# Kernel optimization log

Measured on AMD Instinct MI355X. Metric: run time of the kernel, lower is better.

Reference implementation:

```python
import jax, jax.numpy as jnp
import numpy as np

N_NODES = 50000
DROP_P = 0.2


def gcn_conv(x, edge_index, W, b):
    """PyG GCNConv: add self-loops, symmetric D^-1/2 (A+I) D^-1/2 normalization."""
    n = x.shape[0]
    loop = jnp.arange(n, dtype=edge_index.dtype)
    src = jnp.concatenate([edge_index[0], loop])  # [E+N]
    dst = jnp.concatenate([edge_index[1], loop])  # [E+N]
    # degree over destination (incl. self loop), all edge weights = 1
    deg = jax.ops.segment_sum(jnp.ones_like(src, dtype=x.dtype), dst, num_segments=n)
    dinv = jnp.where(deg > 0, jax.lax.rsqrt(deg), 0.0)
    norm = dinv[src] * dinv[dst]  # [E+N]
    h = x @ W  # [N, F_out] transform first (PyG order)
    msg = h[src] * norm[:, None]  # gather + scale
    out = jax.ops.segment_sum(msg, dst, num_segments=n)  # scatter-add
    return out + b


def setup_inputs() -> dict:
    key = jax.random.key(0)
    ks = jax.random.split(key, 4)
    x = jax.random.normal(ks[0], (N_NODES, 512), dtype=jnp.float32)
    edge_index = jax.random.randint(ks[1], (2, 800000), 0, N_NODES, dtype=jnp.int64)
    W1 = jax.random.normal(ks[2], (512, 256), dtype=jnp.float32) * (1.0 / np.sqrt(512))
    b1 = jnp.zeros((256,), dtype=jnp.float32)
    W2 = jax.random.normal(ks[3], (256, 128), dtype=jnp.float32) * (1.0 / np.sqrt(256))
    b2 = jnp.zeros((128,), dtype=jnp.float32)
    return {"x": x, "edge_index": edge_index, "W1": W1, "b1": b1, "W2": W2, "b2": b2}


def reference(x, edge_index, W1, b1, W2, b2):
    h = gcn_conv(x, edge_index, W1, b1)
    h = jax.nn.relu(h)
    # F.dropout(p=0.2) with training=True default; deterministic fixed-key mask
    keep = jax.random.bernoulli(jax.random.key(42), 1.0 - DROP_P, h.shape)
    h = jnp.where(keep, h / (1.0 - DROP_P), 0.0)
    h = gcn_conv(h, edge_index, W2, b2)
    return jax.nn.softmax(h, axis=1)
```

## Files before the change

kernel.cpp:

```cpp
#include <hip/hip_runtime.h>
#include <stdint.h>

#define N_NODES 50000
#define N_EDGES 800000
#define F0 512
#define F1 256
#define F2 128
#define CAP 64

typedef __attribute__((ext_vector_type(8))) short short8;
typedef __attribute__((ext_vector_type(4))) float float4v;

__device__ __forceinline__ uint32_t r8_rotl(uint32_t x, int r) {
    return (x << r) | (x >> (32 - r));
}

__device__ __forceinline__ uint32_t r8_bits32(uint32_t idx) {
    const uint32_t ks0 = 0u;
    const uint32_t ks1 = 42u;
    const uint32_t ks2 = 0x1BD11BDAu ^ ks0 ^ ks1;
    uint32_t x0 = ks0;
    uint32_t x1 = idx + ks1;
#define R8R(r) { x0 += x1; x1 = r8_rotl(x1, (r)); x1 ^= x0; }
    R8R(13) R8R(15) R8R(26) R8R(6)
    x0 += ks1; x1 += ks2 + 1u;
    R8R(17) R8R(29) R8R(16) R8R(24)
    x0 += ks2; x1 += ks0 + 2u;
    R8R(13) R8R(15) R8R(26) R8R(6)
    x0 += ks0; x1 += ks1 + 3u;
    R8R(17) R8R(29) R8R(16) R8R(24)
    x0 += ks1; x1 += ks2 + 4u;
    R8R(13) R8R(15) R8R(26) R8R(6)
    x0 += ks2; x1 += ks0 + 5u;
#undef R8R
    return x0 ^ x1;
}

__device__ __forceinline__ int r8_keep(uint32_t idx) {
    return (r8_bits32(idx) >> 9) < 0x666667u;
}

__device__ __forceinline__ unsigned short r8_f2bf(float f) {
    uint32_t u = __float_as_uint(f);
    uint32_t r = u + 0x7fffu + ((u >> 16) & 1u);
    return (unsigned short)(r >> 16);
}

__global__ void r8_detect(const uint32_t* __restrict__ ei, int* __restrict__ flag) {
    int t = threadIdx.x;
    uint32_t v = ei[2 * t + 1] | ei[128 + 2 * t + 1];
    unsigned long long any_nonzero = __ballot(v != 0u);
    if (t == 0) flag[0] = (any_nonzero == 0ull) ? 1 : 0;
}

__global__ void r8_fill(const int* __restrict__ ei, const int* __restrict__ flag,
                        int* __restrict__ cursor, int* __restrict__ bucket) {
    int e = blockIdx.x * 256 + threadIdx.x;
    if (e < N_EDGES) {
        int f = flag[0];
        int s = ei[(size_t)e << f];
        int d = ei[(size_t)(N_EDGES + e) << f];
        int pos = atomicAdd(&cursor[d], 1);
        if (pos < CAP) bucket[(size_t)d * CAP + pos] = s;
    }
}

__global__ void r8_dinv(const int* __restrict__ cursor, float* __restrict__ dinv) {
    int v = blockIdx.x * 256 + threadIdx.x;
    if (v < N_NODES) dinv[v] = 1.0f / sqrtf((float)(cursor[v] + 1));
}

__global__ void r8_w1t(const float* __restrict__ W1, unsigned short* __restrict__ Bt) {
    int k = blockIdx.x;
    int n = threadIdx.x;
    Bt[(size_t)n * F0 + k] = r8_f2bf(W1[(size_t)k * F1 + n]);
}

__global__ void r8_w2t(const float* __restrict__ W2, unsigned short* __restrict__ Bt) {
    int k = blockIdx.x;
    int n = threadIdx.x;
    Bt[(size_t)n * F1 + k] = r8_f2bf(W2[(size_t)k * F2 + n]);
}

#define G1_LDA 40
__global__ __launch_bounds__(512)
void r8_gemm1(const float* __restrict__ A, const unsigned short* __restrict__ Bt,
              unsigned short* __restrict__ C, int M) {
    __shared__ unsigned short As[2][128][G1_LDA];
    __shared__ unsigned short Bs[2][256][G1_LDA];
    const int bm = blockIdx.x * 128;
    const int tid = threadIdx.x;
    const int wave = tid >> 6;
    const int lane = tid & 63;
    const int wm = (wave & 1) * 64;
    const int wn = (wave >> 1) * 64;
    const int l15 = lane & 15;
    const int quad = lane >> 4;

    const int asr = tid >> 2;
    const int ask = (tid & 3) * 8;
    const int bsr = tid >> 1;
    const int bsk = (tid & 1) * 16;

    float4v acc[4][4];
#pragma unroll
    for (int i = 0; i < 4; ++i)
#pragma unroll
        for (int j = 0; j < 4; ++j) acc[i][j] = (float4v){0.f, 0.f, 0.f, 0.f};

    const int arow = bm + asr;
    const bool avalid = arow < M;
    const float* aptr = A + (size_t)(avalid ? arow : 0) * F0 + ask;
    const unsigned short* bptr = Bt + (size_t)bsr * F0 + bsk;

    float4 apfA[2], apfB[2];
    short8 bpfA[2], bpfB[2];
#pragma unroll
    for (int q = 0; q < 2; ++q) {
        apfA[q] = make_float4(0.f, 0.f, 0.f, 0.f);
        apfB[q] = make_float4(0.f, 0.f, 0.f, 0.f);
    }

    auto load_tile = [&](int kt, float4 (&apf)[2], short8 (&bpf)[2]) {
        const int k0 = kt * 32;
        if (avalid) {
            const float4* ap = (const float4*)(aptr + k0);
            apf[0] = ap[0];
            apf[1] = ap[1];
        }
        bpf[0] = *(const short8*)(bptr + k0);
        bpf[1] = *(const short8*)(bptr + k0 + 8);
    };

    auto write_buf = [&](int buf, const float4 (&apf)[2], const short8 (&bpf)[2]) {
        union { short8 v; unsigned short u[8]; } t;
        t.u[0] = r8_f2bf(apf[0].x); t.u[1] = r8_f2bf(apf[0].y);
        t.u[2] = r8_f2bf(apf[0].z); t.u[3] = r8_f2bf(apf[0].w);
        t.u[4] = r8_f2bf(apf[1].x); t.u[5] = r8_f2bf(apf[1].y);
        t.u[6] = r8_f2bf(apf[1].z); t.u[7] = r8_f2bf(apf[1].w);
        *(short8*)&As[buf][asr][ask] = t.v;
        *(short8*)&Bs[buf][bsr][bsk] = bpf[0];
        *(short8*)&Bs[buf][bsr][bsk + 8] = bpf[1];
    };

    auto compute = [&](int cur) {
        short8 afr[4], bfr[4];
#pragma unroll
        for (int mi = 0; mi < 4; ++mi)
            afr[mi] = *(const short8*)&As[cur][wm + mi * 16 + l15][quad * 8];
#pragma unroll
        for (int ni = 0; ni < 4; ++ni)
            bfr[ni] = *(const short8*)&Bs[cur][wn + ni * 16 + l15][quad * 8];
#pragma unroll
        for (int mi = 0; mi < 4; ++mi)
#pragma unroll
            for (int ni = 0; ni < 4; ++ni)
                acc[mi][ni] = __builtin_amdgcn_mfma_f32_16x16x32_bf16(
                    afr[mi], bfr[ni], acc[mi][ni], 0, 0, 0);
    };

    const int NT = F0 / 32;
    load_tile(0, apfA, bpfA);
    write_buf(0, apfA, bpfA);
    load_tile(1, apfB, bpfB);
    __syncthreads();

    for (int kt = 0; kt < NT; kt += 2) {
        if (kt + 2 < NT) load_tile(kt + 2, apfA, bpfA);
        compute(0);
        write_buf(1, apfB, bpfB);
        __syncthreads();
        if (kt + 3 < NT) load_tile(kt + 3, apfB, bpfB);
        compute(1);
        if (kt + 2 < NT) write_buf(0, apfA, bpfA);
        __syncthreads();
    }

#pragma unroll
    for (int mi = 0; mi < 4; ++mi) {
#pragma unroll
        for (int r = 0; r < 4; ++r) {
            int row = bm + wm + mi * 16 + quad * 4 + r;
            if (row < M) {
                unsigned short* cp = C + (size_t)row * F1 + wn + l15;
#pragma unroll
                for (int ni = 0; ni < 4; ++ni) cp[ni * 16] = r8_f2bf(acc[mi][ni][r]);
            }
        }
    }
}

#define G2_LDA 40
__global__ __launch_bounds__(256)
void r8_gemm2(const unsigned short* __restrict__ A, const unsigned short* __restrict__ Bt,
              unsigned short* __restrict__ C, int M) {
    __shared__ unsigned short As[2][64][G2_LDA];
    __shared__ unsigned short Bs[2][128][G2_LDA];
    const int bm = blockIdx.x * 64;
    const int tid = threadIdx.x;
    const int wave = tid >> 6;
    const int lane = tid & 63;
    const int wm = (wave & 1) * 32;
    const int wn = (wave >> 1) * 64;
    const int l15 = lane & 15;
    const int quad = lane >> 4;

    const int asr = tid >> 2;
    const int ask = (tid & 3) * 8;
    const int bsr = tid >> 1;
    const int bsk = (tid & 1) * 16;

    float4v acc[2][4];
#pragma unroll
    for (int i = 0; i < 2; ++i)
#pragma unroll
        for (int j = 0; j < 4; ++j) acc[i][j] = (float4v){0.f, 0.f, 0.f, 0.f};

    const int arow = bm + asr;
    const bool avalid = arow < M;
    const unsigned short* aptr = A + (size_t)(avalid ? arow : 0) * F1 + ask;
    const unsigned short* bptr = Bt + (size_t)bsr * F1 + bsk;

    short8 apfA = (short8){0,0,0,0,0,0,0,0}, apfB = (short8){0,0,0,0,0,0,0,0};
    short8 bpfA[2], bpfB[2];

    auto load_tile = [&](int kt, short8& apf, short8 (&bpf)[2]) {
        const int k0 = kt * 32;
        if (avalid) apf = *(const short8*)(aptr + k0);
        bpf[0] = *(const short8*)(bptr + k0);
        bpf[1] = *(const short8*)(bptr + k0 + 8);
    };

    auto write_buf = [&](int buf, const short8& apf, const short8 (&bpf)[2]) {
        *(short8*)&As[buf][asr][ask] = apf;
        *(short8*)&Bs[buf][bsr][bsk] = bpf[0];
        *(short8*)&Bs[buf][bsr][bsk + 8] = bpf[1];
    };

    auto compute = [&](int cur) {
        short8 afr[2], bfr[4];
#pragma unroll
        for (int mi = 0; mi < 2; ++mi)
            afr[mi] = *(const short8*)&As[cur][wm + mi * 16 + l15][quad * 8];
#pragma unroll
        for (int ni = 0; ni < 4; ++ni)
            bfr[ni] = *(const short8*)&Bs[cur][wn + ni * 16 + l15][quad * 8];
#pragma unroll
        for (int mi = 0; mi < 2; ++mi)
#pragma unroll
            for (int ni = 0; ni < 4; ++ni)
                acc[mi][ni] = __builtin_amdgcn_mfma_f32_16x16x32_bf16(
                    afr[mi], bfr[ni], acc[mi][ni], 0, 0, 0);
    };

    const int NT = F1 / 32;
    load_tile(0, apfA, bpfA);
    write_buf(0, apfA, bpfA);
    load_tile(1, apfB, bpfB);
    __syncthreads();

    for (int kt = 0; kt < NT; kt += 2) {
        if (kt + 2 < NT) load_tile(kt + 2, apfA, bpfA);
        compute(0);
        write_buf(1, apfB, bpfB);
        __syncthreads();
        if (kt + 3 < NT) load_tile(kt + 3, apfB, bpfB);
        compute(1);
        if (kt + 2 < NT) write_buf(0, apfA, bpfA);
        __syncthreads();
    }

#pragma unroll
    for (int mi = 0; mi < 2; ++mi) {
#pragma unroll
        for (int r = 0; r < 4; ++r) {
            int row = bm + wm + mi * 16 + quad * 4 + r;
            if (row < M) {
                unsigned short* cp = C + (size_t)row * F2 + wn + l15;
#pragma unroll
                for (int ni = 0; ni < 4; ++ni) cp[ni * 16] = r8_f2bf(acc[mi][ni][r]);
            }
        }
    }
}

__global__ __launch_bounds__(256)
void r8_prop1(const unsigned short* __restrict__ h1, const int* __restrict__ bucket,
              const int* __restrict__ deg, const float* __restrict__ dinv,
              const float* __restrict__ b1, unsigned short* __restrict__ a1) {
    const int v = (blockIdx.x << 2) + (threadIdx.x >> 6);
    const int lane = threadIdx.x & 63;
    const float dv = dinv[v];
    int cnt = deg[v]; if (cnt > CAP) cnt = CAP;

    int s_l = 0; float w_l = 0.f;
    if (lane < cnt) {
        s_l = bucket[(size_t)v * CAP + lane];
        w_l = dinv[s_l] * dv;
    }

    const unsigned short* hrow = h1 + (size_t)lane * 4;
    uint2 hq = *(const uint2*)(h1 + (size_t)v * F1 + lane * 4);
    const float w0 = dv * dv;
    float ax = __uint_as_float(hq.x << 16) * w0;
    float ay = __uint_as_float(hq.x & 0xffff0000u) * w0;
    float az = __uint_as_float(hq.y << 16) * w0;
    float aw = __uint_as_float(hq.y & 0xffff0000u) * w0;

    for (int j = 0; j < cnt; j += 8) {
        int   s[8];
        float w[8];
#pragma unroll
        for (int u = 0; u < 8; ++u) {
            s[u] = __shfl(s_l, j + u);
            w[u] = __shfl(w_l, j + u);
        }
        uint2 r[8];
#pragma unroll
        for (int u = 0; u < 8; ++u)
            r[u] = *(const uint2*)(hrow + (size_t)s[u] * F1);
#pragma unroll
        for (int u = 0; u < 8; ++u) {
            ax += __uint_as_float(r[u].x << 16) * w[u];
            ay += __uint_as_float(r[u].x & 0xffff0000u) * w[u];
            az += __uint_as_float(r[u].y << 16) * w[u];
            aw += __uint_as_float(r[u].y & 0xffff0000u) * w[u];
        }
    }

    float4 bb = *(const float4*)(b1 + lane * 4);
    ax = fmaxf(ax + bb.x, 0.f);
    ay = fmaxf(ay + bb.y, 0.f);
    az = fmaxf(az + bb.z, 0.f);
    aw = fmaxf(aw + bb.w, 0.f);
    uint32_t idx = (uint32_t)v * F1 + (uint32_t)lane * 4;
    ax = r8_keep(idx + 0) ? ax * 1.25f : 0.0f;
    ay = r8_keep(idx + 1) ? ay * 1.25f : 0.0f;
    az = r8_keep(idx + 2) ? az * 1.25f : 0.0f;
    aw = r8_keep(idx + 3) ? aw * 1.25f : 0.0f;
    uint2 st;
    st.x = (uint32_t)r8_f2bf(ax) | ((uint32_t)r8_f2bf(ay) << 16);
    st.y = (uint32_t)r8_f2bf(az) | ((uint32_t)r8_f2bf(aw) << 16);
    *(uint2*)(a1 + (size_t)v * F1 + lane * 4) = st;
}

__global__ __launch_bounds__(256)
void r8_prop2(const unsigned short* __restrict__ h2, const int* __restrict__ bucket,
              const int* __restrict__ deg, const float* __restrict__ dinv,
              const float* __restrict__ b2, float* __restrict__ out) {
    const int v = (blockIdx.x << 2) + (threadIdx.x >> 6);
    const int lane = threadIdx.x & 63;
    const float dv = dinv[v];
    int cnt = deg[v]; if (cnt > CAP) cnt = CAP;

    int s_l = 0; float w_l = 0.f;
    if (lane < cnt) {
        s_l = bucket[(size_t)v * CAP + lane];
        w_l = dinv[s_l] * dv;
    }

    const unsigned short* hrow = h2 + (size_t)lane * 2;
    uint32_t hq = *(const uint32_t*)(h2 + (size_t)v * F2 + lane * 2);
    const float w0 = dv * dv;
    float ax = __uint_as_float(hq << 16) * w0;
    float ay = __uint_as_float(hq & 0xffff0000u) * w0;

    for (int j = 0; j < cnt; j += 8) {
        int   s[8];
        float w[8];
#pragma unroll
        for (int u = 0; u < 8; ++u) {
            s[u] = __shfl(s_l, j + u);
            w[u] = __shfl(w_l, j + u);
        }
        uint32_t r[8];
#pragma unroll
        for (int u = 0; u < 8; ++u)
            r[u] = *(const uint32_t*)(hrow + (size_t)s[u] * F2);
#pragma unroll
        for (int u = 0; u < 8; ++u) {
            ax += __uint_as_float(r[u] << 16) * w[u];
            ay += __uint_as_float(r[u] & 0xffff0000u) * w[u];
        }
    }

    float2 bb = *(const float2*)(b2 + lane * 2);
    ax += bb.x; ay += bb.y;
    float m = fmaxf(ax, ay);
#pragma unroll
    for (int o = 32; o >= 1; o >>= 1) m = fmaxf(m, __shfl_xor(m, o, 64));
    float ex = expf(ax - m), ey = expf(ay - m);
    float s = ex + ey;
#pragma unroll
    for (int o = 32; o >= 1; o >>= 1) s += __shfl_xor(s, o, 64);
    float inv = 1.0f / s;
    *(float2*)(out + (size_t)v * F2 + lane * 2) = make_float2(ex * inv, ey * inv);
}

extern "C" void kernel_launch(void* const* d_in, const int* in_sizes, int n_in,
                              void* d_out, int out_size, void* d_ws, size_t ws_size,
                              hipStream_t stream) {
    const float* x  = (const float*)d_in[0];
    const int*   ei = (const int*)d_in[1];
    const float* W1 = (const float*)d_in[2];
    const float* b1 = (const float*)d_in[3];
    const float* W2 = (const float*)d_in[4];
    const float* b2 = (const float*)d_in[5];
    float* out = (float*)d_out;

    char* ws = (char*)d_ws;
    size_t o = 0;
    auto alloc = [&](size_t bytes) -> char* {
        char* p = ws + o;
        o += (bytes + 511) & ~(size_t)511;
        return p;
    };
    int*            flag   = (int*)           alloc(4);
    int*            cursor = (int*)           alloc((size_t)N_NODES * 4);
    float*          dinv   = (float*)         alloc((size_t)N_NODES * 4);
    int*            bucket = (int*)           alloc((size_t)N_NODES * CAP * 4);
    unsigned short* w1t    = (unsigned short*)alloc((size_t)F1 * F0 * 2);
    unsigned short* w2t    = (unsigned short*)alloc((size_t)F2 * F1 * 2);
    unsigned short* h1     = (unsigned short*)alloc((size_t)N_NODES * F1 * 2);
    unsigned short* a1     = (unsigned short*)alloc((size_t)N_NODES * F1 * 2);
    unsigned short* h2     = (unsigned short*)alloc((size_t)N_NODES * F2 * 2);

    hipMemsetAsync(cursor, 0, (size_t)N_NODES * 4, stream);
    r8_detect<<<1, 64, 0, stream>>>((const uint32_t*)ei, flag);
    r8_fill<<<(N_EDGES + 255) / 256, 256, 0, stream>>>(ei, flag, cursor, bucket);
    r8_dinv<<<(N_NODES + 255) / 256, 256, 0, stream>>>(cursor, dinv);
    r8_w1t<<<F0, F1, 0, stream>>>(W1, w1t);
    r8_w2t<<<F1, F2, 0, stream>>>(W2, w2t);

    r8_gemm1<<<(N_NODES + 127) / 128, 512, 0, stream>>>(x, w1t, h1, N_NODES);

    r8_prop1<<<N_NODES / 4, 256, 0, stream>>>(h1, bucket, cursor, dinv, b1, a1);

    r8_gemm2<<<(N_NODES + 63) / 64, 256, 0, stream>>>(a1, w2t, h2, N_NODES);

    r8_prop2<<<N_NODES / 4, 256, 0, stream>>>(h2, bucket, cursor, dinv, b2, out);
}
```

Baseline: 345.7 us.

## Fuse layer-1 propagation with second GEMM through shared memory

Merges the first aggregation kernel and the second GEMM into one kernel. Each 512-thread block aggregates 16 nodes into a shared-memory tile of post-dropout activations, then runs bf16 MFMA against W2 to write h2 directly. This drops the a1 intermediate (a global write and re-read) and one launch. In exchange, each block re-reads the W2 tile from global/L2 and the aggregation and GEMM phases are serialised within the block.

```diff
diff --git a/kernel.cpp b/kernel.cpp
--- a/kernel.cpp
+++ b/kernel.cpp
@@ -190,158 +190,91 @@
     }
 }
 
-#define G2_LDA 40
-__global__ __launch_bounds__(256)
-void r8_gemm2(const unsigned short* __restrict__ A, const unsigned short* __restrict__ Bt,
-              unsigned short* __restrict__ C, int M) {
-    __shared__ unsigned short As[2][64][G2_LDA];
-    __shared__ unsigned short Bs[2][128][G2_LDA];
-    const int bm = blockIdx.x * 64;
+#define P1_LDA 264
+__global__ __launch_bounds__(512)
+void r8_prop1g2(const unsigned short* __restrict__ h1, const int* __restrict__ bucket,
+                const int* __restrict__ deg, const float* __restrict__ dinv,
+                const float* __restrict__ b1, const unsigned short* __restrict__ w2t,
+                unsigned short* __restrict__ h2) {
+    __shared__ unsigned short a1s[16][P1_LDA];
     const int tid = threadIdx.x;
     const int wave = tid >> 6;
     const int lane = tid & 63;
-    const int wm = (wave & 1) * 32;
-    const int wn = (wave >> 1) * 64;
+    const int nbase = blockIdx.x * 16;
+
+    for (int i = 0; i < 2; ++i) {
+        const int lrow = wave * 2 + i;
+        const int v = nbase + lrow;
+        const float dv = dinv[v];
+        int cnt = deg[v]; if (cnt > CAP) cnt = CAP;
+
+        int s_l = 0; float w_l = 0.f;
+        if (lane < cnt) {
+            s_l = bucket[(size_t)v * CAP + lane];
+            w_l = dinv[s_l] * dv;
+        }
+
+        const unsigned short* hrow = h1 + (size_t)lane * 4;
+        uint2 hq = *(const uint2*)(h1 + (size_t)v * F1 + lane * 4);
+        const float w0 = dv * dv;
+        float ax = __uint_as_float(hq.x << 16) * w0;
+        float ay = __uint_as_float(hq.x & 0xffff0000u) * w0;
+        float az = __uint_as_float(hq.y << 16) * w0;
+        float aw = __uint_as_float(hq.y & 0xffff0000u) * w0;
+
+        for (int j = 0; j < cnt; j += 8) {
+            int   s[8];
+            float w[8];
+#pragma unroll
+            for (int u = 0; u < 8; ++u) {
+                s[u] = __shfl(s_l, j + u);
+                w[u] = __shfl(w_l, j + u);
+            }
+            uint2 r[8];
+#pragma unroll
+            for (int u = 0; u < 8; ++u)
+                r[u] = *(const uint2*)(hrow + (size_t)s[u] * F1);
+#pragma unroll
+            for (int u = 0; u < 8; ++u) {
+                ax += __uint_as_float(r[u].x << 16) * w[u];
+                ay += __uint_as_float(r[u].x & 0xffff0000u) * w[u];
+                az += __uint_as_float(r[u].y << 16) * w[u];
+                aw += __uint_as_float(r[u].y & 0xffff0000u) * w[u];
+            }
+        }
+
+        float4 bb = *(const float4*)(b1 + lane * 4);
+        ax = fmaxf(ax + bb.x, 0.f);
+        ay = fmaxf(ay + bb.y, 0.f);
+        az = fmaxf(az + bb.z, 0.f);
+        aw = fmaxf(aw + bb.w, 0.f);
+        uint32_t idx = (uint32_t)v * F1 + (uint32_t)lane * 4;
+        ax = r8_keep(idx + 0) ? ax * 1.25f : 0.0f;
+        ay = r8_keep(idx + 1) ? ay * 1.25f : 0.0f;
+        az = r8_keep(idx + 2) ? az * 1.25f : 0.0f;
+        aw = r8_keep(idx + 3) ? aw * 1.25f : 0.0f;
+        uint2 st;
+        st.x = (uint32_t)r8_f2bf(ax) | ((uint32_t)r8_f2bf(ay) << 16);
+        st.y = (uint32_t)r8_f2bf(az) | ((uint32_t)r8_f2bf(aw) << 16);
+        *(uint2*)&a1s[lrow][lane * 4] = st;
+    }
+
+    __syncthreads();
+
     const int l15 = lane & 15;
     const int quad = lane >> 4;
-
-    const int asr = tid >> 2;
-    const int ask = (tid & 3) * 8;
-    const int bsr = tid >> 1;
-    const int bsk = (tid & 1) * 16;
-
-    float4v acc[2][4];
-#pragma unroll
-    for (int i = 0; i < 2; ++i)
-#pragma unroll
-        for (int j = 0; j < 4; ++j) acc[i][j] = (float4v){0.f, 0.f, 0.f, 0.f};
-
-    const int arow = bm + asr;
-    const bool avalid = arow < M;
-    const unsigned short* aptr = A + (size_t)(avalid ? arow : 0) * F1 + ask;
-    const unsigned short* bptr = Bt + (size_t)bsr * F1 + bsk;
-
-    short8 apfA = (short8){0,0,0,0,0,0,0,0}, apfB = (short8){0,0,0,0,0,0,0,0};
-    short8 bpfA[2], bpfB[2];
-
-    auto load_tile = [&](int kt, short8& apf, short8 (&bpf)[2]) {
-        const int k0 = kt * 32;
-        if (avalid) apf = *(const short8*)(aptr + k0);
-        bpf[0] = *(const short8*)(bptr + k0);
-        bpf[1] = *(const short8*)(bptr + k0 + 8);
-    };
-
-    auto write_buf = [&](int buf, const short8& apf, const short8 (&bpf)[2]) {
-        *(short8*)&As[buf][asr][ask] = apf;
-        *(short8*)&Bs[buf][bsr][bsk] = bpf[0];
-        *(short8*)&Bs[buf][bsr][bsk + 8] = bpf[1];
-    };
-
-    auto compute = [&](int cur) {
-        short8 afr[2], bfr[4];
-#pragma unroll
-        for (int mi = 0; mi < 2; ++mi)
-            afr[mi] = *(const short8*)&As[cur][wm + mi * 16 + l15][quad * 8];
-#pragma unroll
-        for (int ni = 0; ni < 4; ++ni)
-            bfr[ni] = *(const short8*)&Bs[cur][wn + ni * 16 + l15][quad * 8];
-#pragma unroll
-        for (int mi = 0; mi < 2; ++mi)
-#pragma unroll
-            for (int ni = 0; ni < 4; ++ni)
-                acc[mi][ni] = __builtin_amdgcn_mfma_f32_16x16x32_bf16(
-                    afr[mi], bfr[ni], acc[mi][ni], 0, 0, 0);
-    };
-
-    const int NT = F1 / 32;
-    load_tile(0, apfA, bpfA);
-    write_buf(0, apfA, bpfA);
-    load_tile(1, apfB, bpfB);
-    __syncthreads();
-
-    for (int kt = 0; kt < NT; kt += 2) {
-        if (kt + 2 < NT) load_tile(kt + 2, apfA, bpfA);
-        compute(0);
-        write_buf(1, apfB, bpfB);
-        __syncthreads();
-        if (kt + 3 < NT) load_tile(kt + 3, apfB, bpfB);
-        compute(1);
-        if (kt + 2 < NT) write_buf(0, apfA, bpfA);
-        __syncthreads();
-    }
-
-#pragma unroll
-    for (int mi = 0; mi < 2; ++mi) {
-#pragma unroll
-        for (int r = 0; r < 4; ++r) {
-            int row = bm + wm + mi * 16 + quad * 4 + r;
-            if (row < M) {
-                unsigned short* cp = C + (size_t)row * F2 + wn + l15;
-#pragma unroll
-                for (int ni = 0; ni < 4; ++ni) cp[ni * 16] = r8_f2bf(acc[mi][ni][r]);
-            }
-        }
-    }
-}
-
-__global__ __launch_bounds__(256)
-void r8_prop1(const unsigned short* __restrict__ h1, const int* __restrict__ bucket,
-              const int* __restrict__ deg, const float* __restrict__ dinv,
-              const float* __restrict__ b1, unsigned short* __restrict__ a1) {
-    const int v = (blockIdx.x << 2) + (threadIdx.x >> 6);
-    const int lane = threadIdx.x & 63;
-    const float dv = dinv[v];
-    int cnt = deg[v]; if (cnt > CAP) cnt = CAP;
-
-    int s_l = 0; float w_l = 0.f;
-    if (lane < cnt) {
-        s_l = bucket[(size_t)v * CAP + lane];
-        w_l = dinv[s_l] * dv;
-    }
-
-    const unsigned short* hrow = h1 + (size_t)lane * 4;
-    uint2 hq = *(const uint2*)(h1 + (size_t)v * F1 + lane * 4);
-    const float w0 = dv * dv;
-    float ax = __uint_as_float(hq.x << 16) * w0;
-    float ay = __uint_as_float(hq.x & 0xffff0000u) * w0;
-    float az = __uint_as_float(hq.y << 16) * w0;
-    float aw = __uint_as_float(hq.y & 0xffff0000u) * w0;
-
-    for (int j = 0; j < cnt; j += 8) {
-        int   s[8];
-        float w[8];
-#pragma unroll
-        for (int u = 0; u < 8; ++u) {
-            s[u] = __shfl(s_l, j + u);
-            w[u] = __shfl(w_l, j + u);
-        }
-        uint2 r[8];
-#pragma unroll
-        for (int u = 0; u < 8; ++u)
-            r[u] = *(const uint2*)(hrow + (size_t)s[u] * F1);
-#pragma unroll
-        for (int u = 0; u < 8; ++u) {
-            ax += __uint_as_float(r[u].x << 16) * w[u];
-            ay += __uint_as_float(r[u].x & 0xffff0000u) * w[u];
-            az += __uint_as_float(r[u].y << 16) * w[u];
-            aw += __uint_as_float(r[u].y & 0xffff0000u) * w[u];
-        }
-    }
-
-    float4 bb = *(const float4*)(b1 + lane * 4);
-    ax = fmaxf(ax + bb.x, 0.f);
-    ay = fmaxf(ay + bb.y, 0.f);
-    az = fmaxf(az + bb.z, 0.f);
-    aw = fmaxf(aw + bb.w, 0.f);
-    uint32_t idx = (uint32_t)v * F1 + (uint32_t)lane * 4;
-    ax = r8_keep(idx + 0) ? ax * 1.25f : 0.0f;
-    ay = r8_keep(idx + 1) ? ay * 1.25f : 0.0f;
-    az = r8_keep(idx + 2) ? az * 1.25f : 0.0f;
-    aw = r8_keep(idx + 3) ? aw * 1.25f : 0.0f;
-    uint2 st;
-    st.x = (uint32_t)r8_f2bf(ax) | ((uint32_t)r8_f2bf(ay) << 16);
-    st.y = (uint32_t)r8_f2bf(az) | ((uint32_t)r8_f2bf(aw) << 16);
-    *(uint2*)(a1 + (size_t)v * F1 + lane * 4) = st;
+    float4v acc = (float4v){0.f, 0.f, 0.f, 0.f};
+    const unsigned short* bp = w2t + (size_t)(wave * 16 + l15) * F1 + quad * 8;
+#pragma unroll
+    for (int k = 0; k < F1; k += 32) {
+        short8 afr = *(const short8*)&a1s[l15][k + quad * 8];
+        short8 bfr = *(const short8*)(bp + k);
+        acc = __builtin_amdgcn_mfma_f32_16x16x32_bf16(afr, bfr, acc, 0, 0, 0);
+    }
+#pragma unroll
+    for (int r = 0; r < 4; ++r) {
+        h2[(size_t)(nbase + quad * 4 + r) * F2 + wave * 16 + l15] = r8_f2bf(acc[r]);
+    }
 }
 
 __global__ __launch_bounds__(256)
@@ -422,7 +355,6 @@
     unsigned short* w1t    = (unsigned short*)alloc((size_t)F1 * F0 * 2);
     unsigned short* w2t    = (unsigned short*)alloc((size_t)F2 * F1 * 2);
     unsigned short* h1     = (unsigned short*)alloc((size_t)N_NODES * F1 * 2);
-    unsigned short* a1     = (unsigned short*)alloc((size_t)N_NODES * F1 * 2);
     unsigned short* h2     = (unsigned short*)alloc((size_t)N_NODES * F2 * 2);
 
     hipMemsetAsync(cursor, 0, (size_t)N_NODES * 4, stream);
@@ -434,9 +366,7 @@
 
     r8_gemm1<<<(N_NODES + 127) / 128, 512, 0, stream>>>(x, w1t, h1, N_NODES);
 
-    r8_prop1<<<N_NODES / 4, 256, 0, stream>>>(h1, bucket, cursor, dinv, b1, a1);
-
-    r8_gemm2<<<(N_NODES + 63) / 64, 256, 0, stream>>>(a1, w2t, h2, N_NODES);
+    r8_prop1g2<<<N_NODES / 16, 512, 0, stream>>>(h1, bucket, cursor, dinv, b1, w2t, h2);
 
     r8_prop2<<<N_NODES / 4, 256, 0, stream>>>(h2, bucket, cursor, dinv, b2, out);
 }
```

Result: slower. 355.4 us (+2.8%).
